# Performance work log

Hardware: AMD Instinct MI355X
Metric: run time of the kernel (lower is better)

## Reference

```python
import jax, jax.numpy as jnp
import numpy as np

DEPTH = 7  # complete binary trees with 2**DEPTH = 128 leaves

B, L = 4096, 128
V, E, OUT = 100000, 128, 3


def setup_inputs() -> dict:
    key = jax.random.key(0)
    ks = jax.random.split(key, 6)
    tokens = jax.random.randint(ks[0], (B, L), 0, V, dtype=jnp.int64)
    embedding = jax.random.normal(ks[1], (V, E), dtype=jnp.float32)
    # tree_layer: Linear(2E -> E); torch stores weight as [out, in]
    W_tree = jax.random.normal(ks[2], (E, 2 * E), dtype=jnp.float32) * (1.0 / np.sqrt(2 * E))
    b_tree = jax.random.normal(ks[3], (E,), dtype=jnp.float32) * 0.01
    # classifier_layer: Linear(E -> OUT)
    W_cls = jax.random.normal(ks[4], (OUT, E), dtype=jnp.float32) * (1.0 / np.sqrt(E))
    b_cls = jax.random.normal(ks[5], (OUT,), dtype=jnp.float32) * 0.01
    return {"tokens": tokens, "embedding": embedding, "W_tree": W_tree,
            "b_tree": b_tree, "W_cls": W_cls, "b_cls": b_cls}


def reference(tokens, embedding, W_tree, b_tree, W_cls, b_cls):
    # Leaf embeddings: gather rows of the embedding table. [B, L, E]
    reps = embedding[tokens]
    # Level-synchronous bottom-up composition (depth-batched across all trees):
    # at each level, pair adjacent nodes, concat features, apply tree_layer + tanh.
    for _ in range(DEPTH):
        left = reps[:, 0::2, :]   # [B, n/2, E]
        right = reps[:, 1::2, :]  # [B, n/2, E]
        combined = jnp.concatenate([left, right], axis=-1)  # [B, n/2, 2E]
        reps = jnp.tanh(jnp.einsum('bnh,eh->bne', combined, W_tree) + b_tree)
    roots = reps[:, 0, :]  # [B, E]
    return roots @ W_cls.T + b_cls  # [B, OUT]
```

## Files before the change

kernel.cpp:

```cpp
#include <hip/hip_runtime.h>
#include <hip/hip_fp16.h>


typedef _Float16 half8 __attribute__((ext_vector_type(8)));
typedef float floatx4 __attribute__((ext_vector_type(4)));

#define STRIDE 264
#define NSAMP 4096

__device__ __forceinline__ float fast_tanh(float x) {
  float cx = fminf(15.f, fmaxf(-15.f, x));
  float e = __expf(2.f * cx);
  return 1.f - 2.f / (e + 1.f);
}

template<int MT>
__device__ __forceinline__ void level_run(
    const _Float16* inb, _Float16* outb, float* rootbuf,
    const half8 (&Wf)[2][8], const float (&bias)[2],
    int Mout, bool writeRoot, int nbase, int l15, int quad)
{
  floatx4 acc[MT][2];
#pragma unroll
  for (int m = 0; m < MT; ++m) {
    acc[m][0] = (floatx4){0.f, 0.f, 0.f, 0.f};
    acc[m][1] = (floatx4){0.f, 0.f, 0.f, 0.f};
  }

#pragma unroll
  for (int m = 0; m < MT; ++m) {
    const _Float16* arow = inb + (m * 16 + l15) * STRIDE + quad * 8;
#pragma unroll
    for (int ks = 0; ks < 8; ++ks) {
      half8 a = *(const half8*)(arow + ks * 32);
      acc[m][0] = __builtin_amdgcn_mfma_f32_16x16x32_f16(a, Wf[0][ks], acc[m][0], 0, 0, 0);
      acc[m][1] = __builtin_amdgcn_mfma_f32_16x16x32_f16(a, Wf[1][ks], acc[m][1], 0, 0, 0);
    }
  }

  const int mrow = quad * 4;
#pragma unroll
  for (int m = 0; m < MT; ++m) {
#pragma unroll
    for (int i = 0; i < 2; ++i) {
      const int col = (nbase + i) * 16 + l15;
      const float b = bias[i];
#pragma unroll
      for (int r = 0; r < 4; ++r) {
        const int node = m * 16 + mrow + r;
        if (node < Mout) {
          float v = fast_tanh(acc[m][i][r] + b);
          if (writeRoot) {
            rootbuf[col] = v;
          } else {
            outb[(node >> 1) * STRIDE + (node & 1) * 128 + col] = (_Float16)v;
          }
        }
      }
    }
  }
}

__global__ __launch_bounds__(256, 3)
void tree_kernel(const int* __restrict__ tokens,
                 const float* __restrict__ embedding,
                 const float* __restrict__ W_tree,
                 const float* __restrict__ b_tree,
                 const float* __restrict__ W_cls,
                 const float* __restrict__ b_cls,
                 float* __restrict__ out)
{
  __shared__ _Float16 bufA[64 * STRIDE];
  __shared__ _Float16 bufB[32 * STRIDE];
  __shared__ float rootbuf[128];

  const int tid  = threadIdx.x;
  const int wid  = tid >> 6;
  const int lane = tid & 63;
  const int l15  = lane & 15;
  const int quad = lane >> 4;
  const int nbase = wid * 2;

  half8 Wf[2][8];
#pragma unroll
  for (int i = 0; i < 2; ++i) {
    const int e = (nbase + i) * 16 + l15;
#pragma unroll
    for (int ks = 0; ks < 8; ++ks) {
      const int k = ks * 32 + quad * 8;
      const float4* p = (const float4*)(W_tree + e * 256 + k);
      float4 lo = p[0], hi = p[1];
      half8 f;
      f[0] = (_Float16)lo.x; f[1] = (_Float16)lo.y; f[2] = (_Float16)lo.z; f[3] = (_Float16)lo.w;
      f[4] = (_Float16)hi.x; f[5] = (_Float16)hi.y; f[6] = (_Float16)hi.z; f[7] = (_Float16)hi.w;
      Wf[i][ks] = f;
    }
  }
  float bias[2];
#pragma unroll
  for (int i = 0; i < 2; ++i) bias[i] = b_tree[(nbase + i) * 16 + l15];

#pragma unroll 1
  for (int s = blockIdx.x; s < NSAMP; s += gridDim.x) {

    {
      const int leaf = tid >> 1;
      const int hh = tid & 1;
      const int tok = tokens[s * 128 + leaf];
      const float4* src = (const float4*)(embedding + (size_t)tok * 128 + hh * 64);
      _Float16* dst = bufA + (leaf >> 1) * STRIDE + (leaf & 1) * 128 + hh * 64;
#pragma unroll
      for (int j = 0; j < 8; ++j) {
        float4 x = src[2 * j];
        float4 y = src[2 * j + 1];
        half8 h;
        h[0] = (_Float16)x.x; h[1] = (_Float16)x.y; h[2] = (_Float16)x.z; h[3] = (_Float16)x.w;
        h[4] = (_Float16)y.x; h[5] = (_Float16)y.y; h[6] = (_Float16)y.z; h[7] = (_Float16)y.w;
        *(half8*)(dst + j * 8) = h;
      }
    }
    __syncthreads();

    level_run<4>(bufA, bufB, rootbuf, Wf, bias, 64, false, nbase, l15, quad);
    __syncthreads();
    level_run<2>(bufB, bufA, rootbuf, Wf, bias, 32, false, nbase, l15, quad);
    __syncthreads();
    level_run<1>(bufA, bufB, rootbuf, Wf, bias, 16, false, nbase, l15, quad);
    __syncthreads();
    level_run<1>(bufB, bufA, rootbuf, Wf, bias,  8, false, nbase, l15, quad);
    __syncthreads();
    level_run<1>(bufA, bufB, rootbuf, Wf, bias,  4, false, nbase, l15, quad);
    __syncthreads();
    level_run<1>(bufB, bufA, rootbuf, Wf, bias,  2, false, nbase, l15, quad);
    __syncthreads();
    level_run<1>(bufA, bufB, rootbuf, Wf, bias,  1, true,  nbase, l15, quad);
    __syncthreads();

    if (wid == 0) {
      const float r0 = rootbuf[lane];
      const float r1 = rootbuf[lane + 64];
#pragma unroll
      for (int o = 0; o < 3; ++o) {
        float p = r0 * W_cls[o * 128 + lane] + r1 * W_cls[o * 128 + 64 + lane];
#pragma unroll
        for (int sh = 32; sh > 0; sh >>= 1) p += __shfl_down(p, sh, 64);
        if (lane == 0) out[s * 3 + o] = p + b_cls[o];
      }
    }
  }
}

extern "C" void kernel_launch(void* const* d_in, const int* in_sizes, int n_in,
                              void* d_out, int out_size, void* d_ws, size_t ws_size,
                              hipStream_t stream) {
  const int*   tokens    = (const int*)d_in[0];
  const float* embedding = (const float*)d_in[1];
  const float* W_tree    = (const float*)d_in[2];
  const float* b_tree    = (const float*)d_in[3];
  const float* W_cls     = (const float*)d_in[4];
  const float* b_cls     = (const float*)d_in[5];
  float* out = (float*)d_out;

  dim3 grid(768), block(256);
  tree_kernel<<<grid, block, 0, stream>>>(tokens, embedding, W_tree, b_tree, W_cls, b_cls, out);
}
```

Before: 182.4 us.

## Prefetch next sample's embeddings into registers during tree compute

Loads the next sample's leaf embedding rows into 16 float4 registers per thread while the current sample's tree levels run, so gather latency overlaps the MFMA work. It also swaps the fp16 conversion to packed round-toward-zero cvt_pkrtz and simplifies tanh by dropping the clamp and using a hardware reciprocal. The 64 extra VGPRs may lower occupancy under launch_bounds(256,3). Round-toward-zero slightly changes numerics.

```diff
diff --git a/kernel.cpp b/kernel.cpp
--- a/kernel.cpp
+++ b/kernel.cpp
@@ -9,9 +9,13 @@
 #define NSAMP 4096
 
 __device__ __forceinline__ float fast_tanh(float x) {
-  float cx = fminf(15.f, fmaxf(-15.f, x));
-  float e = __expf(2.f * cx);
-  return 1.f - 2.f / (e + 1.f);
+  float e = __expf(2.f * x);
+  return 1.f - 2.f * __builtin_amdgcn_rcpf(e + 1.f);
+}
+
+__device__ __forceinline__ unsigned pkrtz(float a, float b) {
+  auto h = __builtin_amdgcn_cvt_pkrtz(a, b);
+  return __builtin_bit_cast(unsigned, h);
 }
 
 template<int MT>
@@ -100,24 +104,39 @@
 #pragma unroll
   for (int i = 0; i < 2; ++i) bias[i] = b_tree[(nbase + i) * 16 + l15];
 
+  const int leaf = tid >> 1;
+  const int hh   = tid & 1;
+  float4 pf[16];
+
+  {
+    const int tok = tokens[blockIdx.x * 128 + leaf];
+    const float4* src = (const float4*)(embedding + (size_t)tok * 128 + hh * 64);
+#pragma unroll
+    for (int j = 0; j < 16; ++j) pf[j] = src[j];
+  }
+
 #pragma unroll 1
   for (int s = blockIdx.x; s < NSAMP; s += gridDim.x) {
 
     {
-      const int leaf = tid >> 1;
-      const int hh = tid & 1;
-      const int tok = tokens[s * 128 + leaf];
-      const float4* src = (const float4*)(embedding + (size_t)tok * 128 + hh * 64);
-      _Float16* dst = bufA + (leaf >> 1) * STRIDE + (leaf & 1) * 128 + hh * 64;
+      uint4* dst = (uint4*)bufA + (leaf >> 1) * 33 + (leaf & 1) * 16 + hh * 8;
 #pragma unroll
       for (int j = 0; j < 8; ++j) {
-        float4 x = src[2 * j];
-        float4 y = src[2 * j + 1];
-        half8 h;
-        h[0] = (_Float16)x.x; h[1] = (_Float16)x.y; h[2] = (_Float16)x.z; h[3] = (_Float16)x.w;
-        h[4] = (_Float16)y.x; h[5] = (_Float16)y.y; h[6] = (_Float16)y.z; h[7] = (_Float16)y.w;
-        *(half8*)(dst + j * 8) = h;
+        float4 x = pf[2 * j], y = pf[2 * j + 1];
+        uint4 w;
+        w.x = pkrtz(x.x, x.y); w.y = pkrtz(x.z, x.w);
+        w.z = pkrtz(y.x, y.y); w.w = pkrtz(y.z, y.w);
+        dst[j] = w;
       }
+    }
+
+    {
+      int snext = s + gridDim.x;
+      if (snext >= NSAMP) snext = s;
+      const int tok = tokens[snext * 128 + leaf];
+      const float4* src = (const float4*)(embedding + (size_t)tok * 128 + hh * 64);
+#pragma unroll
+      for (int j = 0; j < 16; ++j) pf[j] = src[j];
     }
     __syncthreads();
 
```

New measurement: 194.2 us. +6.4%, slower.
